# Performance work log

Measured on AMD Instinct MI355X. Metric: run time of the kernel, lower is better.

Reference implementation:

```python
import jax, jax.numpy as jnp
import numpy as np

B, T, D = 4, 4096, 1024
H, E, K, SPAN = 16, 8, 2, 64
GATE_H = 128


def setup_inputs() -> dict:
    key = jax.random.key(0)
    ks = jax.random.split(key, 7)
    s = 0.02
    return {
        "hidden_states": jax.random.normal(ks[0], (B, T, D), jnp.float32),
        "attention_mask": jnp.ones((B, T), jnp.int32),
        # expert weights, torch Linear convention: y = x @ W.T, W: (out, in)
        "Wq": jax.random.normal(ks[1], (E, D, D), jnp.float32) * s,
        "Wk": jax.random.normal(ks[2], (E, D, D), jnp.float32) * s,
        "Wv": jax.random.normal(ks[3], (E, D, D), jnp.float32) * s,
        "gate_w1": jax.random.normal(ks[4], (GATE_H, D), jnp.float32) * s,
        "gate_b1": jnp.zeros((GATE_H,), jnp.float32),
        "gate_w2": jax.random.normal(ks[5], (E, GATE_H), jnp.float32) * s,
        "gate_b2": jnp.zeros((E,), jnp.float32),
    }


def reference(hidden_states, attention_mask, Wq, Wk, Wv, gate_w1, gate_b1, gate_w2, gate_b2):
    b, t, c = hidden_states.shape
    n_spans = t // SPAN  # T divisible by span_len, full mask -> even split
    hd = c // H
    x = hidden_states.reshape(b, n_spans, SPAN, c)            # (B,S,L,C)
    m = attention_mask.reshape(b, n_spans, SPAN).astype(jnp.float32)

    # masked mean-pool per span
    pooled = (x * m[..., None]).sum(2) / jnp.clip(m.sum(2), 1e-9)[..., None]  # (B,S,C)

    # gating MLP + top-k sparse softmax weights
    h = jax.nn.relu(pooled @ gate_w1.T + gate_b1)
    logits = h @ gate_w2.T + gate_b2                          # (B,S,E)
    vals, idx = jax.lax.top_k(logits, K)
    sm = jax.nn.softmax(vals, axis=-1)
    gw = (jax.nn.one_hot(idx, E, dtype=sm.dtype) * sm[..., None]).sum(-2)  # (B,S,E)

    def combine(W):
        # sum_j gw[...,j] * (x @ W_j.T); small fixed loop over experts
        out = jnp.zeros_like(x)
        for j in range(E):
            out = out + gw[:, :, j][:, :, None, None] * jnp.einsum('bsld,fd->bslf', x, W[j])
        return out

    def heads(z):
        return z.reshape(b, n_spans, SPAN, H, hd).transpose(0, 1, 3, 2, 4)  # (B,S,H,L,hd)

    Qh = heads(combine(Wq))
    Kh = heads(combine(Wk))
    Vh = heads(combine(Wv))

    scores = jnp.einsum('bshld,bshmd->bshlm', Qh, Kh) / jnp.sqrt(jnp.float32(hd))
    mb = (m > 0)[:, :, None, None, :]                         # mask keys
    scores = jnp.where(mb, scores, jnp.finfo(scores.dtype).min)
    probs = jax.nn.softmax(scores, axis=-1)                    # dropout=0 (eval)
    ctx = jnp.einsum('bshlm,bshmd->bshld', probs, Vh)
    out = ctx.transpose(0, 1, 3, 2, 4).reshape(b, t, c)
    return out
```

## Files before the change

### kernel.cpp

```cpp
#include <hip/hip_runtime.h>
#include <hip/hip_bf16.h>

constexpr int Bc = 4, Tc = 4096, Dc = 1024, Hc = 16, Ec = 8;
constexpr int SPANc = 64, NSc = 64, HDc = 64, GHc = 128;
constexpr int NSPAN = 256;
constexpr int MAXMT = 134;
constexpr int NTILES = 12;
constexpr int NSLOT = MAXMT * 4;
#define FINF_MIN (-3.402823466e38f)

typedef __attribute__((ext_vector_type(8))) _Float16 half8;
typedef __attribute__((ext_vector_type(4))) _Float16 half4;
typedef __attribute__((ext_vector_type(4))) float f32x4;

#define LD4(p) (*reinterpret_cast<const float4*>(p))
#define MFMA16(A, B, C) __builtin_amdgcn_mfma_f32_16x16x32_f16(A, B, C, 0, 0, 0)

constexpr size_t WS_UT_OFF = 65536;
constexpr size_t WS_NEED = WS_UT_OFF + (size_t)NSLOT * 3072 * 64 * 2;

__global__ __launch_bounds__(256) void gate_kernel(
    const float* __restrict__ x, const int* __restrict__ mask,
    const float* __restrict__ w1, const float* __restrict__ b1,
    const float* __restrict__ w2, const float* __restrict__ b2,
    int* __restrict__ eidx, float* __restrict__ egw)
{
  const int span = blockIdx.x;
  const int b = span / NSc, s = span % NSc;
  const int tid = threadIdx.x;

  __shared__ float mv[SPANc];
  __shared__ float msum_s;
  __shared__ float pooled[Dc];
  __shared__ float hbuf[GHc];
  __shared__ float logits[Ec];

  if (tid < SPANc) mv[tid] = (float)mask[(size_t)b * Tc + s * SPANc + tid];
  __syncthreads();
  if (tid == 0) {
    float ms = 0.f;
    for (int l = 0; l < SPANc; ++l) ms += mv[l];
    msum_s = fmaxf(ms, 1e-9f);
  }
  __syncthreads();

  {
    const int c0 = tid * 4;
    float a0 = 0.f, a1 = 0.f, a2 = 0.f, a3 = 0.f;
    const float* xb = x + ((size_t)b * Tc + s * SPANc) * Dc + c0;
    for (int l = 0; l < SPANc; ++l) {
      const float m = mv[l];
      const float4 v = *reinterpret_cast<const float4*>(xb + (size_t)l * Dc);
      a0 += v.x * m; a1 += v.y * m; a2 += v.z * m; a3 += v.w * m;
    }
    const float inv = 1.f / msum_s;
    pooled[c0 + 0] = a0 * inv; pooled[c0 + 1] = a1 * inv;
    pooled[c0 + 2] = a2 * inv; pooled[c0 + 3] = a3 * inv;
  }
  __syncthreads();

  if (tid < GHc) {
    const float* wr = w1 + (size_t)tid * Dc;
    float acc = b1[tid];
    for (int c = 0; c < Dc; c += 4) {
      const float4 w = *reinterpret_cast<const float4*>(wr + c);
      acc += pooled[c] * w.x + pooled[c + 1] * w.y + pooled[c + 2] * w.z + pooled[c + 3] * w.w;
    }
    hbuf[tid] = fmaxf(acc, 0.f);
  }
  __syncthreads();

  if (tid < Ec) {
    const float* wr = w2 + tid * GHc;
    float acc = b2[tid];
    for (int j = 0; j < GHc; ++j) acc += hbuf[j] * wr[j];
    logits[tid] = acc;
  }
  __syncthreads();

  if (tid == 0) {
    int e0 = 0; float v0 = logits[0];
    for (int e = 1; e < Ec; ++e) { if (logits[e] > v0) { v0 = logits[e]; e0 = e; } }
    int e1 = (e0 == 0) ? 1 : 0; float v1 = logits[e1];
    for (int e = 0; e < Ec; ++e) {
      if (e == e0 || e == e1) continue;
      if (logits[e] > v1) { v1 = logits[e]; e1 = e; }
    }
    const float ex = expf(v1 - v0);
    const float den = 1.f + ex;
    eidx[span * 2 + 0] = e0; eidx[span * 2 + 1] = e1;
    egw[span * 2 + 0] = 1.f / den; egw[span * 2 + 1] = ex / den;
  }
}

__global__ __launch_bounds__(64) void bookkeep_kernel(
    const int* __restrict__ eidx, int* __restrict__ slotidx,
    int* __restrict__ nmt, int* __restrict__ mtiles)
{
  __shared__ int lists[Ec][NSPAN];
  __shared__ int lslot[Ec][NSPAN];
  __shared__ int cnt[Ec];
  __shared__ int base[Ec + 1];
  const int tid = threadIdx.x;

  if (tid < Ec) {
    int c = 0;
    for (int s = 0; s < NSPAN; ++s) {
      for (int j = 0; j < 2; ++j) {
        if (eidx[s * 2 + j] == tid) { lists[tid][c] = s; lslot[tid][c] = j; ++c; }
      }
    }
    cnt[tid] = c;
  }
  __syncthreads();
  if (tid == 0) {
    int acc = 0;
    for (int e = 0; e < Ec; ++e) { base[e] = acc; acc += (cnt[e] + 3) >> 2; }
    base[Ec] = acc;
    *nmt = acc;
  }
  __syncthreads();
  if (tid < Ec) {
    const int e = tid, c = cnt[e], ng = (c + 3) >> 2;
    for (int g = 0; g < ng; ++g) {
      const int m = base[e] + g;
      mtiles[m * 8 + 0] = e;
      for (int i = 0; i < 4; ++i) {
        const int li = g * 4 + i;
        const int src = (li < c) ? li : 0;
        mtiles[m * 8 + 1 + i] = lists[e][src];
        if (li < c) slotidx[lists[e][li] * 2 + lslot[e][li]] = m * 4 + i;
      }
    }
  }
}

__global__ __launch_bounds__(512, 2) void moe_gemm_kernel(
    const float* __restrict__ x,
    const float* __restrict__ Wq, const float* __restrict__ Wk,
    const float* __restrict__ Wv,
    const int* __restrict__ nmt, const int* __restrict__ mtiles,
    _Float16* __restrict__ Ut)
{
  const int lin = blockIdx.x + gridDim.x * blockIdx.y;
  const int lin2 = (lin & 7) * 201 + (lin >> 3);
  const int mt = lin2 % MAXMT;
  const int nt = lin2 / MAXMT;
  if (mt >= *nmt) return;

  const int e = mtiles[mt * 8 + 0];
  int spans[4];
#pragma unroll
  for (int i = 0; i < 4; ++i) spans[i] = mtiles[mt * 8 + 1 + i];

  const int mat = nt >> 2;
  const int wcol0 = (nt & 3) * 256;
  const float* Wp = (mat == 0) ? Wq : (mat == 1) ? Wk : Wv;
  const float* Wbase = Wp + ((size_t)e * Dc + wcol0) * Dc;

  __shared__ _Float16 As[256][36];
  __shared__ _Float16 Bs[256][36];

  const int t = threadIdx.x;
  const int arow = t >> 1;
  const int acol0 = (t & 1) * 16;
  const float* asrc = x + ((size_t)spans[arow >> 6] * SPANc + (arow & 63)) * Dc + acol0;
  const float* bsrc = Wbase + (size_t)arow * Dc + acol0;

  const int w = t >> 6, lane = t & 63;
  const int lr = lane & 15, koff = (lane >> 4) * 8;
  const int rbase = (w >> 2) * 128;
  const int cbase = (w & 3) * 64;

  f32x4 acc[8][4];
#pragma unroll
  for (int ri = 0; ri < 8; ++ri)
#pragma unroll
    for (int ci = 0; ci < 4; ++ci)
#pragma unroll
      for (int j = 0; j < 4; ++j) acc[ri][ci][j] = 0.f;

  float4 pa0 = LD4(asrc), pa1 = LD4(asrc + 4), pa2 = LD4(asrc + 8), pa3 = LD4(asrc + 12);
  float4 pb0 = LD4(bsrc), pb1 = LD4(bsrc + 4), pb2 = LD4(bsrc + 8), pb3 = LD4(bsrc + 12);

  for (int k0 = 0; k0 < Dc; k0 += 32) {
    __syncthreads();
    {
      half8 ha, hb;
      ha[0] = (_Float16)pa0.x; ha[1] = (_Float16)pa0.y;
      ha[2] = (_Float16)pa0.z; ha[3] = (_Float16)pa0.w;
      ha[4] = (_Float16)pa1.x; ha[5] = (_Float16)pa1.y;
      ha[6] = (_Float16)pa1.z; ha[7] = (_Float16)pa1.w;
      *reinterpret_cast<half8*>(&As[arow][acol0]) = ha;
      ha[0] = (_Float16)pa2.x; ha[1] = (_Float16)pa2.y;
      ha[2] = (_Float16)pa2.z; ha[3] = (_Float16)pa2.w;
      ha[4] = (_Float16)pa3.x; ha[5] = (_Float16)pa3.y;
      ha[6] = (_Float16)pa3.z; ha[7] = (_Float16)pa3.w;
      *reinterpret_cast<half8*>(&As[arow][acol0 + 8]) = ha;
      hb[0] = (_Float16)(pb0.x * 64.f); hb[1] = (_Float16)(pb0.y * 64.f);
      hb[2] = (_Float16)(pb0.z * 64.f); hb[3] = (_Float16)(pb0.w * 64.f);
      hb[4] = (_Float16)(pb1.x * 64.f); hb[5] = (_Float16)(pb1.y * 64.f);
      hb[6] = (_Float16)(pb1.z * 64.f); hb[7] = (_Float16)(pb1.w * 64.f);
      *reinterpret_cast<half8*>(&Bs[arow][acol0]) = hb;
      hb[0] = (_Float16)(pb2.x * 64.f); hb[1] = (_Float16)(pb2.y * 64.f);
      hb[2] = (_Float16)(pb2.z * 64.f); hb[3] = (_Float16)(pb2.w * 64.f);
      hb[4] = (_Float16)(pb3.x * 64.f); hb[5] = (_Float16)(pb3.y * 64.f);
      hb[6] = (_Float16)(pb3.z * 64.f); hb[7] = (_Float16)(pb3.w * 64.f);
      *reinterpret_cast<half8*>(&Bs[arow][acol0 + 8]) = hb;
    }
    if (k0 < Dc - 32) {
      asrc += 32; bsrc += 32;
      pa0 = LD4(asrc); pa1 = LD4(asrc + 4); pa2 = LD4(asrc + 8); pa3 = LD4(asrc + 12);
      pb0 = LD4(bsrc); pb1 = LD4(bsrc + 4); pb2 = LD4(bsrc + 8); pb3 = LD4(bsrc + 12);
      __builtin_amdgcn_sched_barrier(0);
    }
    __syncthreads();

    half8 afr[8], bfr[4];
#pragma unroll
    for (int ri = 0; ri < 8; ++ri)
      afr[ri] = *reinterpret_cast<const half8*>(&As[rbase + ri * 16 + lr][koff]);
#pragma unroll
    for (int ci = 0; ci < 4; ++ci)
      bfr[ci] = *reinterpret_cast<const half8*>(&Bs[cbase + ci * 16 + lr][koff]);
#pragma unroll
    for (int ri = 0; ri < 8; ++ri)
#pragma unroll
      for (int ci = 0; ci < 4; ++ci)
        acc[ri][ci] = MFMA16(afr[ri], bfr[ci], acc[ri][ci]);
  }

#pragma unroll
  for (int ri = 0; ri < 8; ++ri)
#pragma unroll
    for (int ci = 0; ci < 4; ++ci) {
      const int f = wcol0 + cbase + ci * 16 + lr;
      const int row0 = rbase + ri * 16 + (lane >> 4) * 4;
      const int slot = mt * 4 + (row0 >> 6);
      half4 hv;
#pragma unroll
      for (int j = 0; j < 4; ++j) hv[j] = (_Float16)acc[ri][ci][j];
      *reinterpret_cast<half4*>(
          Ut + ((size_t)slot * 3072 + mat * 1024 + f) * 64 + (row0 & 63)) = hv;
    }
}

__global__ __launch_bounds__(256, 3) void attn_kernel(
    const int* __restrict__ mask, const int* __restrict__ slotidx,
    const float* __restrict__ egw, const _Float16* __restrict__ Ut,
    float* __restrict__ out)
{
  const int h = blockIdx.x;
  const int s = blockIdx.y;
  const int b = blockIdx.z;
  const int span = b * NSc + s;
  const int tid = threadIdx.x;

  __shared__ _Float16 Qf[64][68];
  __shared__ _Float16 Kf[64][68];
  __shared__ _Float16 VT[64][68];
  __shared__ _Float16 Pf[64][68];
  __shared__ float    sc[64][68];

  const int sA = slotidx[span * 2 + 0];
  const int sB = slotidx[span * 2 + 1];
  const float gA = egw[span * 2 + 0] * 0.015625f;
  const float gB = egw[span * 2 + 1] * 0.015625f;

  const int d = tid >> 2;
  const int l0 = (tid & 3) * 16;

  for (int mat = 0; mat < 3; ++mat) {
    const _Float16* pa = Ut + ((size_t)sA * 3072 + mat * 1024 + h * HDc + d) * 64 + l0;
    const _Float16* pb = Ut + ((size_t)sB * 3072 + mat * 1024 + h * HDc + d) * 64 + l0;
    const half8 a0 = *reinterpret_cast<const half8*>(pa);
    const half8 a1 = *reinterpret_cast<const half8*>(pa + 8);
    const half8 b0 = *reinterpret_cast<const half8*>(pb);
    const half8 b1 = *reinterpret_cast<const half8*>(pb + 8);
    if (mat == 2) {
      half8 v0, v1;
#pragma unroll
      for (int j = 0; j < 8; ++j) {
        v0[j] = (_Float16)(gA * (float)a0[j] + gB * (float)b0[j]);
        v1[j] = (_Float16)(gA * (float)a1[j] + gB * (float)b1[j]);
      }
      *reinterpret_cast<half8*>(&VT[d][l0]) = v0;
      *reinterpret_cast<half8*>(&VT[d][l0 + 8]) = v1;
    } else if (mat == 0) {
#pragma unroll
      for (int j = 0; j < 8; ++j) {
        Qf[l0 + j][d] = (_Float16)(gA * (float)a0[j] + gB * (float)b0[j]);
        Qf[l0 + 8 + j][d] = (_Float16)(gA * (float)a1[j] + gB * (float)b1[j]);
      }
    } else {
#pragma unroll
      for (int j = 0; j < 8; ++j) {
        Kf[l0 + j][d] = (_Float16)(gA * (float)a0[j] + gB * (float)b0[j]);
        Kf[l0 + 8 + j][d] = (_Float16)(gA * (float)a1[j] + gB * (float)b1[j]);
      }
    }
  }
  __syncthreads();

  const int w = tid >> 6, lane = tid & 63;
  const int lr = lane & 15, koff = (lane >> 4) * 8;
  const int rbase = (w >> 1) * 32, cbase = (w & 1) * 32;

  {
    f32x4 aS[2][2];
#pragma unroll
    for (int mi = 0; mi < 2; ++mi)
#pragma unroll
      for (int ni = 0; ni < 2; ++ni)
#pragma unroll
        for (int j = 0; j < 4; ++j) aS[mi][ni][j] = 0.f;
#pragma unroll
    for (int kc = 0; kc < 64; kc += 32) {
      const half8 a0 = *reinterpret_cast<const half8*>(&Qf[rbase + lr][kc + koff]);
      const half8 a1 = *reinterpret_cast<const half8*>(&Qf[rbase + 16 + lr][kc + koff]);
      const half8 b0 = *reinterpret_cast<const half8*>(&Kf[cbase + lr][kc + koff]);
      const half8 b1 = *reinterpret_cast<const half8*>(&Kf[cbase + 16 + lr][kc + koff]);
      aS[0][0] = MFMA16(a0, b0, aS[0][0]); aS[0][1] = MFMA16(a0, b1, aS[0][1]);
      aS[1][0] = MFMA16(a1, b0, aS[1][0]); aS[1][1] = MFMA16(a1, b1, aS[1][1]);
    }
    const bool kv0 = mask[(size_t)b * Tc + s * SPANc + cbase + lr] != 0;
    const bool kv1 = mask[(size_t)b * Tc + s * SPANc + cbase + 16 + lr] != 0;
#pragma unroll
    for (int mi = 0; mi < 2; ++mi)
#pragma unroll
      for (int ni = 0; ni < 2; ++ni) {
        const int col = cbase + ni * 16 + lr;
        const int row0 = rbase + mi * 16 + (lane >> 4) * 4;
        const bool kv = (ni == 0) ? kv0 : kv1;
#pragma unroll
        for (int j = 0; j < 4; ++j)
          sc[row0 + j][col] = kv ? aS[mi][ni][j] * 0.125f : FINF_MIN;
      }
  }
  __syncthreads();

  if (tid < 64) {
    float mx = FINF_MIN;
    for (int mm = 0; mm < 64; ++mm) {
      const int m = (mm + tid) & 63;
      mx = fmaxf(mx, sc[tid][m]);
    }
    float sum = 0.f;
    for (int mm = 0; mm < 64; ++mm) {
      const int m = (mm + tid) & 63;
      const float e = expf(sc[tid][m] - mx);
      sc[tid][m] = e;
      sum += e;
    }
    const float inv = 1.f / sum;
    for (int mm = 0; mm < 64; ++mm) {
      const int m = (mm + tid) & 63;
      Pf[tid][m] = (_Float16)(sc[tid][m] * inv);
    }
  }
  __syncthreads();

  {
    f32x4 aC[2][2];
#pragma unroll
    for (int mi = 0; mi < 2; ++mi)
#pragma unroll
      for (int ni = 0; ni < 2; ++ni)
#pragma unroll
        for (int j = 0; j < 4; ++j) aC[mi][ni][j] = 0.f;
#pragma unroll
    for (int kc = 0; kc < 64; kc += 32) {
      const half8 a0 = *reinterpret_cast<const half8*>(&Pf[rbase + lr][kc + koff]);
      const half8 a1 = *reinterpret_cast<const half8*>(&Pf[rbase + 16 + lr][kc + koff]);
      const half8 b0 = *reinterpret_cast<const half8*>(&VT[cbase + lr][kc + koff]);
      const half8 b1 = *reinterpret_cast<const half8*>(&VT[cbase + 16 + lr][kc + koff]);
      aC[0][0] = MFMA16(a0, b0, aC[0][0]); aC[0][1] = MFMA16(a0, b1, aC[0][1]);
      aC[1][0] = MFMA16(a1, b0, aC[1][0]); aC[1][1] = MFMA16(a1, b1, aC[1][1]);
    }
    float* ob = out + ((size_t)b * Tc + s * SPANc) * Dc + h * HDc;
#pragma unroll
    for (int mi = 0; mi < 2; ++mi)
#pragma unroll
      for (int ni = 0; ni < 2; ++ni) {
        const int col = cbase + ni * 16 + lr;
        const int row0 = rbase + mi * 16 + (lane >> 4) * 4;
#pragma unroll
        for (int j = 0; j < 4; ++j)
          ob[(size_t)(row0 + j) * Dc + col] = aC[mi][ni][j];
      }
  }
}

__global__ __launch_bounds__(256, 3) void moe_attn_fb(
    const float* __restrict__ x, const int* __restrict__ mask,
    const float* __restrict__ Wq, const float* __restrict__ Wk,
    const float* __restrict__ Wv,
    const int* __restrict__ eidx, const float* __restrict__ egw,
    float* __restrict__ out)
{
  const int h = blockIdx.x;
  const int s = blockIdx.y;
  const int b = blockIdx.z;
  const int span = b * NSc + s;
  const int tid = threadIdx.x;

  __shared__ __align__(16) char smem[52224];
  _Float16* XF  = (_Float16*)(smem);
  _Float16* WHs = (_Float16*)(smem + 5120);
  _Float16* WLs = (_Float16*)(smem + 10240);
  float* qs = (float*)(smem);
  float* ks = (float*)(smem + 17408);
  float* vs = (float*)(smem + 34816);

  const int e0 = eidx[span * 2 + 0];
  const int e1 = eidx[span * 2 + 1];
  const float g0s = egw[span * 2 + 0] * 64.f;
  const float g1s = egw[span * 2 + 1] * 64.f;

  const int lrow = tid >> 2;
  const int kq = (tid & 3) * 8;
  const int stg_off = lrow * 40 + kq;

  const int w = tid >> 6;
  const int lane = tid & 63;
  const int lr = lane & 15;
  const int koff = (lane >> 4) * 8;
  const int rbase = (w >> 1) * 32;
  const int cbase = (w & 1) * 32;

  const float* xb = x + ((size_t)b * Tc + s * SPANc) * Dc;
  const size_t woff0 = ((size_t)e0 * Dc + h * HDc + lrow) * Dc + kq;
  const size_t woff1 = ((size_t)e1 * Dc + h * HDc + lrow) * Dc + kq;

  const float* xcur  = xb + (size_t)lrow * Dc + kq;
  const float* w0cur = Wv + woff0;
  const float* w1cur = Wv + woff1;
  float4 rx0, rx1, ra0, ra1, rb0, rb1;
  rx0 = LD4(xcur); rx1 = LD4(xcur + 4);
  ra0 = LD4(w0cur); ra1 = LD4(w0cur + 4);
  rb0 = LD4(w1cur); rb1 = LD4(w1cur + 4);

  for (int p = 0; p < 3; ++p) {
    f32x4 acc[2][2];
#pragma unroll
    for (int mi = 0; mi < 2; ++mi)
#pragma unroll
      for (int ni = 0; ni < 2; ++ni)
#pragma unroll
        for (int j = 0; j < 4; ++j) acc[mi][ni][j] = 0.f;

    for (int t = 0; t < 32; ++t) {
      __syncthreads();
      {
        half8 hx;
        hx[0] = (_Float16)rx0.x; hx[1] = (_Float16)rx0.y;
        hx[2] = (_Float16)rx0.z; hx[3] = (_Float16)rx0.w;
        hx[4] = (_Float16)rx1.x; hx[5] = (_Float16)rx1.y;
        hx[6] = (_Float16)rx1.z; hx[7] = (_Float16)rx1.w;
        *reinterpret_cast<half8*>(XF + stg_off) = hx;
      }
      {
        float wv[8];
        wv[0] = g0s * ra0.x + g1s * rb0.x; wv[1] = g0s * ra0.y + g1s * rb0.y;
        wv[2] = g0s * ra0.z + g1s * rb0.z; wv[3] = g0s * ra0.w + g1s * rb0.w;
        wv[4] = g0s * ra1.x + g1s * rb1.x; wv[5] = g0s * ra1.y + g1s * rb1.y;
        wv[6] = g0s * ra1.z + g1s * rb1.z; wv[7] = g0s * ra1.w + g1s * rb1.w;
        half8 hw, lw;
#pragma unroll
        for (int i = 0; i < 8; ++i) {
          const _Float16 wh = (_Float16)wv[i];
          hw[i] = wh;
          lw[i] = (_Float16)(wv[i] - (float)wh);
        }
        *reinterpret_cast<half8*>(WHs + stg_off) = hw;
        *reinterpret_cast<half8*>(WLs + stg_off) = lw;
      }
      if (!(p == 2 && t == 31)) {
        if (t < 31) {
          xcur += 32; w0cur += 32; w1cur += 32;
        } else {
          const float* Wn = (p == 0) ? Wk : Wq;
          xcur = xb + (size_t)lrow * Dc + kq;
          w0cur = Wn + woff0;
          w1cur = Wn + woff1;
        }
        rx0 = LD4(xcur); rx1 = LD4(xcur + 4);
        ra0 = LD4(w0cur); ra1 = LD4(w0cur + 4);
        rb0 = LD4(w1cur); rb1 = LD4(w1cur + 4);
      }
      __syncthreads();

      const half8 a0  = *reinterpret_cast<const half8*>(XF  + (rbase + lr) * 40 + koff);
      const half8 a1  = *reinterpret_cast<const half8*>(XF  + (rbase + 16 + lr) * 40 + koff);
      const half8 bh0 = *reinterpret_cast<const half8*>(WHs + (cbase + lr) * 40 + koff);
      const half8 bh1 = *reinterpret_cast<const half8*>(WHs + (cbase + 16 + lr) * 40 + koff);
      const half8 bl0 = *reinterpret_cast<const half8*>(WLs + (cbase + lr) * 40 + koff);
      const half8 bl1 = *reinterpret_cast<const half8*>(WLs + (cbase + 16 + lr) * 40 + koff);

      acc[0][0] = MFMA16(a0, bh0, acc[0][0]);
      acc[0][1] = MFMA16(a0, bh1, acc[0][1]);
      acc[1][0] = MFMA16(a1, bh0, acc[1][0]);
      acc[1][1] = MFMA16(a1, bh1, acc[1][1]);
      acc[0][0] = MFMA16(a0, bl0, acc[0][0]);
      acc[0][1] = MFMA16(a0, bl1, acc[0][1]);
      acc[1][0] = MFMA16(a1, bl0, acc[1][0]);
      acc[1][1] = MFMA16(a1, bl1, acc[1][1]);
    }

    float* dst = (p == 0) ? vs : (p == 1) ? ks : qs;
    if (p == 2) __syncthreads();
#pragma unroll
    for (int mi = 0; mi < 2; ++mi)
#pragma unroll
      for (int ni = 0; ni < 2; ++ni) {
        const int col = cbase + ni * 16 + lr;
        const int row0 = rbase + mi * 16 + (lane >> 4) * 4;
#pragma unroll
        for (int j = 0; j < 4; ++j)
          dst[(row0 + j) * 68 + col] = acc[mi][ni][j] * 0.015625f;
      }
  }
  __syncthreads();

  const int tx = tid & 15;
  const int ty = tid >> 4;
  bool kvalid[4];
#pragma unroll
  for (int j = 0; j < 4; ++j)
    kvalid[j] = mask[(size_t)b * Tc + s * SPANc + tx * 4 + j] != 0;

  float sacc[4][4] = {{0.f, 0.f, 0.f, 0.f}, {0.f, 0.f, 0.f, 0.f},
                      {0.f, 0.f, 0.f, 0.f}, {0.f, 0.f, 0.f, 0.f}};
  for (int dd = 0; dd < 64; ++dd) {
    const int d = (dd + tid) & 63;
    const float a0 = qs[(ty * 4 + 0) * 68 + d], a1 = qs[(ty * 4 + 1) * 68 + d];
    const float a2 = qs[(ty * 4 + 2) * 68 + d], a3 = qs[(ty * 4 + 3) * 68 + d];
    const float b0 = ks[(tx * 4 + 0) * 68 + d], b1v = ks[(tx * 4 + 1) * 68 + d];
    const float b2v = ks[(tx * 4 + 2) * 68 + d], b3 = ks[(tx * 4 + 3) * 68 + d];
    sacc[0][0] += a0 * b0; sacc[0][1] += a0 * b1v; sacc[0][2] += a0 * b2v; sacc[0][3] += a0 * b3;
    sacc[1][0] += a1 * b0; sacc[1][1] += a1 * b1v; sacc[1][2] += a1 * b2v; sacc[1][3] += a1 * b3;
    sacc[2][0] += a2 * b0; sacc[2][1] += a2 * b1v; sacc[2][2] += a2 * b2v; sacc[2][3] += a2 * b3;
    sacc[3][0] += a3 * b0; sacc[3][1] += a3 * b1v; sacc[3][2] += a3 * b2v; sacc[3][3] += a3 * b3;
  }
  __syncthreads();
#pragma unroll
  for (int i = 0; i < 4; ++i)
#pragma unroll
    for (int j = 0; j < 4; ++j)
      qs[(ty * 4 + i) * 68 + tx * 4 + j] = kvalid[j] ? sacc[i][j] * 0.125f : FINF_MIN;
  __syncthreads();

  if (tid < 64) {
    float mx = FINF_MIN;
    for (int mm = 0; mm < 64; ++mm) {
      const int m = (mm + tid) & 63;
      mx = fmaxf(mx, qs[tid * 68 + m]);
    }
    float sum = 0.f;
    for (int mm = 0; mm < 64; ++mm) {
      const int m = (mm + tid) & 63;
      const float e = expf(qs[tid * 68 + m] - mx);
      qs[tid * 68 + m] = e;
      sum += e;
    }
    const float inv = 1.f / sum;
    for (int mm = 0; mm < 64; ++mm) {
      const int m = (mm + tid) & 63;
      qs[tid * 68 + m] *= inv;
    }
  }
  __syncthreads();

  float cacc[4][4] = {{0.f, 0.f, 0.f, 0.f}, {0.f, 0.f, 0.f, 0.f},
                      {0.f, 0.f, 0.f, 0.f}, {0.f, 0.f, 0.f, 0.f}};
  for (int m = 0; m < 64; ++m) {
    const float p0 = qs[(ty * 4 + 0) * 68 + m], p1 = qs[(ty * 4 + 1) * 68 + m];
    const float p2 = qs[(ty * 4 + 2) * 68 + m], p3 = qs[(ty * 4 + 3) * 68 + m];
    const float4 vv = *reinterpret_cast<const float4*>(&vs[m * 68 + tx * 4]);
    cacc[0][0] += p0 * vv.x; cacc[0][1] += p0 * vv.y; cacc[0][2] += p0 * vv.z; cacc[0][3] += p0 * vv.w;
    cacc[1][0] += p1 * vv.x; cacc[1][1] += p1 * vv.y; cacc[1][2] += p1 * vv.z; cacc[1][3] += p1 * vv.w;
    cacc[2][0] += p2 * vv.x; cacc[2][1] += p2 * vv.y; cacc[2][2] += p2 * vv.z; cacc[2][3] += p2 * vv.w;
    cacc[3][0] += p3 * vv.x; cacc[3][1] += p3 * vv.y; cacc[3][2] += p3 * vv.z; cacc[3][3] += p3 * vv.w;
  }

  float* ob = out + ((size_t)b * Tc + s * SPANc) * Dc + h * HDc;
#pragma unroll
  for (int i = 0; i < 4; ++i) {
    *reinterpret_cast<float4*>(ob + (size_t)(ty * 4 + i) * Dc + tx * 4) =
        make_float4(cacc[i][0], cacc[i][1], cacc[i][2], cacc[i][3]);
  }
}

extern "C" void kernel_launch(void* const* d_in, const int* in_sizes, int n_in,
                              void* d_out, int out_size, void* d_ws, size_t ws_size,
                              hipStream_t stream) {
  const float* x   = (const float*)d_in[0];
  const int*   msk = (const int*)d_in[1];
  const float* Wq  = (const float*)d_in[2];
  const float* Wk  = (const float*)d_in[3];
  const float* Wv  = (const float*)d_in[4];
  const float* w1  = (const float*)d_in[5];
  const float* b1  = (const float*)d_in[6];
  const float* w2  = (const float*)d_in[7];
  const float* b2  = (const float*)d_in[8];
  float* out = (float*)d_out;

  char* ws = (char*)d_ws;
  int*   eidx    = (int*)(ws + 0);
  float* egw     = (float*)(ws + 2048);
  int*   slotidx = (int*)(ws + 4096);
  int*   nmt     = (int*)(ws + 6144);
  int*   mtiles  = (int*)(ws + 6208);
  _Float16* Ut   = (_Float16*)(ws + WS_UT_OFF);

  gate_kernel<<<NSPAN, 256, 0, stream>>>(x, msk, w1, b1, w2, b2, eidx, egw);

  if (ws_size >= WS_NEED) {
    bookkeep_kernel<<<1, 64, 0, stream>>>(eidx, slotidx, nmt, mtiles);
    moe_gemm_kernel<<<dim3(MAXMT, NTILES), 512, 0, stream>>>(
        x, Wq, Wk, Wv, nmt, mtiles, Ut);
    attn_kernel<<<dim3(Hc, NSc, Bc), 256, 0, stream>>>(msk, slotidx, egw, Ut, out);
  } else {
    moe_attn_fb<<<dim3(Hc, NSc, Bc), 256, 0, stream>>>(
        x, msk, Wq, Wk, Wv, eidx, egw, out);
  }
}
```

Before: 594.3 us.

## Pre-convert inputs and expert weights to fp16 before the MoE GEMM

Adds a grid-stride conversion kernel that casts x and all three expert weight tensors to fp16 in workspace on every call, with the weights scaled by 64. A new GEMM kernel then loads fp16 tiles directly into shared memory with register prefetch and raised wave priority around the MFMA block, so the main loop no longer loads fp32 and converts per tile. The aim is to halve operand bandwidth and remove conversion work from the GEMM inner loop. In exchange it adds four conversion launches that stream the full weight set, about 96 MB read, plus a larger workspace requirement. The older fp32 path is kept as a fallback when the workspace is too small.

```diff
diff --git a/kernel.cpp b/kernel.cpp
--- a/kernel.cpp
+++ b/kernel.cpp
@@ -1,5 +1,6 @@
 #include <hip/hip_runtime.h>
 #include <hip/hip_bf16.h>
+#include <hip/hip_fp16.h>
 
 constexpr int Bc = 4, Tc = 4096, Dc = 1024, Hc = 16, Ec = 8;
 constexpr int SPANc = 64, NSc = 64, HDc = 64, GHc = 128;
@@ -14,10 +15,39 @@
 typedef __attribute__((ext_vector_type(4))) float f32x4;
 
 #define LD4(p) (*reinterpret_cast<const float4*>(p))
+#define LDU4(p) (*reinterpret_cast<const uint4*>(p))
 #define MFMA16(A, B, C) __builtin_amdgcn_mfma_f32_16x16x32_f16(A, B, C, 0, 0, 0)
 
-constexpr size_t WS_UT_OFF = 65536;
-constexpr size_t WS_NEED = WS_UT_OFF + (size_t)NSLOT * 3072 * 64 * 2;
+constexpr size_t OFF_EIDX = 0;
+constexpr size_t OFF_EGW  = 2048;
+constexpr size_t OFF_SLOT = 4096;
+constexpr size_t OFF_NMT  = 6144;
+constexpr size_t OFF_MT   = 6208;
+constexpr size_t OFF_UT   = 65536;
+constexpr size_t UT_BYTES = (size_t)NSLOT * 3072 * 64 * 2;
+constexpr size_t WS_MID   = OFF_UT + UT_BYTES;
+constexpr size_t OFF_X16  = WS_MID;
+constexpr size_t X16_BYTES = (size_t)Bc * Tc * Dc * 2;
+constexpr size_t OFF_W16  = OFF_X16 + X16_BYTES;
+constexpr size_t W16_BYTES = (size_t)3 * Ec * Dc * Dc * 2;
+constexpr size_t WS_FULL  = OFF_W16 + W16_BYTES;
+
+__global__ __launch_bounds__(256) void cvt16_kernel(
+    const float* __restrict__ src, _Float16* __restrict__ dst, int n8, float scl)
+{
+  int i = blockIdx.x * 256 + threadIdx.x;
+  const int stride = gridDim.x * 256;
+  for (; i < n8; i += stride) {
+    const float4 a = LD4(src + (size_t)i * 8);
+    const float4 b = LD4(src + (size_t)i * 8 + 4);
+    half8 h;
+    h[0] = (_Float16)(a.x * scl); h[1] = (_Float16)(a.y * scl);
+    h[2] = (_Float16)(a.z * scl); h[3] = (_Float16)(a.w * scl);
+    h[4] = (_Float16)(b.x * scl); h[5] = (_Float16)(b.y * scl);
+    h[6] = (_Float16)(b.z * scl); h[7] = (_Float16)(b.w * scl);
+    *reinterpret_cast<half8*>(dst + (size_t)i * 8) = h;
+  }
+}
 
 __global__ __launch_bounds__(256) void gate_kernel(
     const float* __restrict__ x, const int* __restrict__ mask,
@@ -135,7 +165,100 @@
   }
 }
 
-__global__ __launch_bounds__(512, 2) void moe_gemm_kernel(
+__global__ __launch_bounds__(512, 2) void moe_gemm_f16(
+    const _Float16* __restrict__ X16, const _Float16* __restrict__ W16,
+    const int* __restrict__ nmt, const int* __restrict__ mtiles,
+    _Float16* __restrict__ Ut)
+{
+  const int lin = blockIdx.x + gridDim.x * blockIdx.y;
+  const int lin2 = (lin & 7) * 201 + (lin >> 3);
+  const int mt = lin2 % MAXMT;
+  const int nt = lin2 / MAXMT;
+  if (mt >= *nmt) return;
+
+  const int e = mtiles[mt * 8 + 0];
+  int spans[4];
+#pragma unroll
+  for (int i = 0; i < 4; ++i) spans[i] = mtiles[mt * 8 + 1 + i];
+
+  const int mat = nt >> 2;
+  const int wcol0 = (nt & 3) * 256;
+  const _Float16* Wb = W16 + (size_t)mat * ((size_t)Ec * Dc * Dc)
+                     + ((size_t)e * Dc + wcol0) * Dc;
+
+  __shared__ _Float16 As[256][36];
+  __shared__ _Float16 Bs[256][36];
+
+  const int t = threadIdx.x;
+  const int arow = t >> 1;
+  const int acol0 = (t & 1) * 16;
+  const _Float16* asrc = X16 + ((size_t)spans[arow >> 6] * SPANc + (arow & 63)) * Dc + acol0;
+  const _Float16* bsrc = Wb + (size_t)arow * Dc + acol0;
+
+  const int w = t >> 6, lane = t & 63;
+  const int lr = lane & 15, koff = (lane >> 4) * 8;
+  const int rbase = (w >> 2) * 128;
+  const int cbase = (w & 3) * 64;
+
+  f32x4 acc[8][4];
+#pragma unroll
+  for (int ri = 0; ri < 8; ++ri)
+#pragma unroll
+    for (int ci = 0; ci < 4; ++ci)
+#pragma unroll
+      for (int j = 0; j < 4; ++j) acc[ri][ci][j] = 0.f;
+
+  uint4 pa0 = LDU4(asrc), pa1 = LDU4(asrc + 8);
+  uint4 pb0 = LDU4(bsrc), pb1 = LDU4(bsrc + 8);
+
+  for (int k0 = 0; k0 < Dc; k0 += 32) {
+    __syncthreads();
+    {
+      *reinterpret_cast<uint4*>(&As[arow][acol0]) = pa0;
+      *reinterpret_cast<uint4*>(&As[arow][acol0 + 8]) = pa1;
+      *reinterpret_cast<uint4*>(&Bs[arow][acol0]) = pb0;
+      *reinterpret_cast<uint4*>(&Bs[arow][acol0 + 8]) = pb1;
+    }
+    if (k0 < Dc - 32) {
+      asrc += 32; bsrc += 32;
+      pa0 = LDU4(asrc); pa1 = LDU4(asrc + 8);
+      pb0 = LDU4(bsrc); pb1 = LDU4(bsrc + 8);
+      __builtin_amdgcn_sched_barrier(0);
+    }
+    __syncthreads();
+
+    half8 afr[8], bfr[4];
+#pragma unroll
+    for (int ri = 0; ri < 8; ++ri)
+      afr[ri] = *reinterpret_cast<const half8*>(&As[rbase + ri * 16 + lr][koff]);
+#pragma unroll
+    for (int ci = 0; ci < 4; ++ci)
+      bfr[ci] = *reinterpret_cast<const half8*>(&Bs[cbase + ci * 16 + lr][koff]);
+    __builtin_amdgcn_s_setprio(1);
+#pragma unroll
+    for (int ri = 0; ri < 8; ++ri)
+#pragma unroll
+      for (int ci = 0; ci < 4; ++ci)
+        acc[ri][ci] = MFMA16(afr[ri], bfr[ci], acc[ri][ci]);
+    __builtin_amdgcn_s_setprio(0);
+  }
+
+#pragma unroll
+  for (int ri = 0; ri < 8; ++ri)
+#pragma unroll
+    for (int ci = 0; ci < 4; ++ci) {
+      const int f = wcol0 + cbase + ci * 16 + lr;
+      const int row0 = rbase + ri * 16 + (lane >> 4) * 4;
+      const int slot = mt * 4 + (row0 >> 6);
+      half4 hv;
+#pragma unroll
+      for (int j = 0; j < 4; ++j) hv[j] = (_Float16)acc[ri][ci][j];
+      *reinterpret_cast<half4*>(
+          Ut + ((size_t)slot * 3072 + mat * 1024 + f) * 64 + (row0 & 63)) = hv;
+    }
+}
+
+__global__ __launch_bounds__(512, 2) void moe_gemm_f32(
     const float* __restrict__ x,
     const float* __restrict__ Wq, const float* __restrict__ Wk,
     const float* __restrict__ Wv,
@@ -606,18 +729,30 @@
   float* out = (float*)d_out;
 
   char* ws = (char*)d_ws;
-  int*   eidx    = (int*)(ws + 0);
-  float* egw     = (float*)(ws + 2048);
-  int*   slotidx = (int*)(ws + 4096);
-  int*   nmt     = (int*)(ws + 6144);
-  int*   mtiles  = (int*)(ws + 6208);
-  _Float16* Ut   = (_Float16*)(ws + WS_UT_OFF);
+  int*      eidx    = (int*)(ws + OFF_EIDX);
+  float*    egw     = (float*)(ws + OFF_EGW);
+  int*      slotidx = (int*)(ws + OFF_SLOT);
+  int*      nmt     = (int*)(ws + OFF_NMT);
+  int*      mtiles  = (int*)(ws + OFF_MT);
+  _Float16* Ut      = (_Float16*)(ws + OFF_UT);
+  _Float16* X16     = (_Float16*)(ws + OFF_X16);
+  _Float16* W16     = (_Float16*)(ws + OFF_W16);
 
   gate_kernel<<<NSPAN, 256, 0, stream>>>(x, msk, w1, b1, w2, b2, eidx, egw);
 
-  if (ws_size >= WS_NEED) {
+  if (ws_size >= WS_FULL) {
     bookkeep_kernel<<<1, 64, 0, stream>>>(eidx, slotidx, nmt, mtiles);
-    moe_gemm_kernel<<<dim3(MAXMT, NTILES), 512, 0, stream>>>(
+    const int nW8 = Ec * Dc * Dc / 8;
+    const int nX8 = Bc * Tc * Dc / 8;
+    cvt16_kernel<<<1024, 256, 0, stream>>>(Wq, W16, nW8, 64.f);
+    cvt16_kernel<<<1024, 256, 0, stream>>>(Wk, W16 + (size_t)Ec * Dc * Dc, nW8, 64.f);
+    cvt16_kernel<<<1024, 256, 0, stream>>>(Wv, W16 + (size_t)2 * Ec * Dc * Dc, nW8, 64.f);
+    cvt16_kernel<<<1024, 256, 0, stream>>>(x, X16, nX8, 1.f);
+    moe_gemm_f16<<<dim3(MAXMT, NTILES), 512, 0, stream>>>(X16, W16, nmt, mtiles, Ut);
+    attn_kernel<<<dim3(Hc, NSc, Bc), 256, 0, stream>>>(msk, slotidx, egw, Ut, out);
+  } else if (ws_size >= WS_MID) {
+    bookkeep_kernel<<<1, 64, 0, stream>>>(eidx, slotidx, nmt, mtiles);
+    moe_gemm_f32<<<dim3(MAXMT, NTILES), 512, 0, stream>>>(
         x, Wq, Wk, Wv, nmt, mtiles, Ut);
     attn_kernel<<<dim3(Hc, NSc, Bc), 256, 0, stream>>>(msk, slotidx, egw, Ut, out);
   } else {
```

Result: no change. 595.8 us (+0.3%).
